# Optimization experiments

Measured on AMD Instinct MI355X. Metric: run time of the kernel, lower is better.

## Reference

```python
import jax, jax.numpy as jnp
import numpy as np

# Model dims (match init_kwargs)
D, L = 64, 262144          # data_size
G, J = 8, 8                # number of relations, dims per relation
FG = 16                    # filters (kernel_size) per relation
W = 31                     # window_size
PAD1 = (W - 1) // 2        # 15, left padding in the original code
F = G * FG                 # 128 total filters


def setup_inputs() -> dict:
    key = jax.random.key(0)
    k1, k2 = jax.random.split(key)
    x = jax.random.normal(k1, (D, L), dtype=jnp.float32)
    # original uses torch.rand for Parameter init -> uniform [0,1)
    params = jax.random.uniform(k2, (G, FG, J, W), dtype=jnp.float32)
    # dim_relation = [[0..7],[8..15],...,[56..63]] == arange reshaped
    rel_idx = jnp.arange(G * J, dtype=jnp.int32).reshape(G, J)
    return {"x": x, "params": params, "rel_idx": rel_idx}


def _forward(x, params, rel_idx):
    xg = x[rel_idx]                                   # [G, J, L] gather relation dims

    # Interior positions (PAD1 <= k <= L-W+PAD1): full-window correlation.
    # Expressed as a grouped 1D conv (lax conv is cross-correlation, matching
    # the original data*kernel elementwise-sum, no kernel flip).
    lhs = xg.reshape(1, G * J, L)                     # [N=1, C=G*J, L]
    rhs = params.reshape(G * FG, J, W)                # [O=G*FG, I=J, W]
    y = jax.lax.conv_general_dilated(
        lhs, rhs, window_strides=(1,),
        padding=[(PAD1, W - 1 - PAD1)],
        dimension_numbers=("NCH", "OIH", "NCH"),
        feature_group_count=G,
    )[0].reshape(G, FG, L)

    # Left boundary (k < PAD1): the original aligns kernel[0] with x[...,0]
    # and truncates BOTH at k+W-PAD1, i.e. y[k] = sum_{w < k+W-PAD1} xg[:, :, w]*K[..., w]
    # (NOT zero padding). Cumulative sum over w gives all prefixes at once.
    pl = jnp.einsum("gjw,gfjw->gfw", xg[:, :, :W], params)      # [G, FG, W]
    left_c = jnp.cumsum(pl, axis=-1)
    y = y.at[:, :, :PAD1].set(left_c[:, :, W - PAD1 - 1: W - 1])

    # Right boundary (k > L-W+PAD1): kernel[-1] aligned with x[..., L-1],
    # truncated at the front: y[k] = sum_{w >= W-m} xg[:, :, L-W+w]*K[..., w],
    # with m = L-k+PAD1. Reverse cumsum gives all suffixes.
    pr = jnp.einsum("gjw,gfjw->gfw", xg[:, :, L - W:], params)  # [G, FG, W]
    right_c = jnp.cumsum(pr[:, :, ::-1], axis=-1)[:, :, ::-1]    # suffix sums
    n_right = W - 1 - PAD1                                       # positions k = L-W+PAD1+1 .. L-1
    y = y.at[:, :, L - n_right:].set(right_c[:, :, 1: W - PAD1])

    return y.reshape(F * L, 1)                        # matches y.view(-1, 1)


def reference(x, params, rel_idx):
    return _forward(x, params, rel_idx)
```

## Files before the change

kernel.cpp:

```cpp
#include <hip/hip_runtime.h>

#define LL    262144
#define GG    8
#define JJ    8
#define FGF   16
#define WW    31
#define PAD1  15
#define NB    1024
#define NTHR  256
#define XTLEN (NB + 32)

typedef __bf16 bf16x8 __attribute__((ext_vector_type(8)));
typedef float  f32x4  __attribute__((ext_vector_type(4)));

__device__ inline unsigned short f2bf(float f) {
    unsigned int u = __float_as_uint(f);
    u = (u + 0x7FFF + ((u >> 16) & 1)) >> 16;
    return (unsigned short)u;
}

__global__ __launch_bounds__(NTHR, 4)
void conv_mfma(const float* __restrict__ x, const float* __restrict__ p,
               const int* __restrict__ rel, float* __restrict__ out)
{
    __shared__ unsigned short pw[32 * 16 * 8];
    __shared__ unsigned short xt[XTLEN * 8];

    const int t = threadIdx.x;
    const int g = blockIdx.y;
    const long nbase = (long)blockIdx.x * NB;

    {
        const float* pg = p + (long)g * FGF * JJ * WW;
        for (int i = t; i < FGF * JJ * WW; i += NTHR) {
            int f = i / (JJ * WW);
            int r = i - f * (JJ * WW);
            int j = r / WW;
            int w = r - j * WW;
            pw[(w * 16 + f) * 8 + j] = f2bf(pg[i]);
        }
        if (t < FGF * JJ) {
            int f = t >> 3, j = t & 7;
            pw[(31 * 16 + f) * 8 + j] = 0;
        }
    }

    {
        const int j  = t >> 5;
        const int p0 = t & 31;
        const float* xr = x + (long)rel[g * JJ + j] * LL;
        #pragma unroll
        for (int c = 0; c < XTLEN / 32; ++c) {
            int pos = c * 32 + p0;
            long gp = nbase - 16 + pos;
            float v = (gp >= 0 && gp < LL) ? xr[gp] : 0.0f;
            xt[pos * 8 + j] = f2bf(v);
        }
    }
    __syncthreads();

    const int lane = t & 63;
    const int wid  = t >> 6;
    const int col  = lane & 15;
    const int q    = lane >> 4;

    bf16x8 a[8];
    #pragma unroll
    for (int s = 0; s < 8; ++s)
        a[s] = *(const bf16x8*)&pw[((s * 4 + q) * 16 + col) * 8];

    const int pb = wid * 256 + col + q + 1;

    #define LDX(pos) (*(const bf16x8*)&xt[(pos) * 8])

    bf16x8 F00 = LDX(pb + 0), F01 = LDX(pb + 4), F02 = LDX(pb + 8), F03 = LDX(pb + 12);

    #pragma unroll
    for (int u = 0; u < 8; ++u) {
        const int o = pb + u * 32;
        bf16x8 F10 = LDX(o + 16), F11 = LDX(o + 20), F12 = LDX(o + 24), F13 = LDX(o + 28);
        bf16x8 F20 = LDX(o + 32), F21 = LDX(o + 36), F22 = LDX(o + 40), F23 = LDX(o + 44);

        f32x4 acc0 = {0.f, 0.f, 0.f, 0.f};
        f32x4 acc1 = {0.f, 0.f, 0.f, 0.f};
        acc0 = __builtin_amdgcn_mfma_f32_16x16x32_bf16(a[0], F00, acc0, 0, 0, 0);
        acc1 = __builtin_amdgcn_mfma_f32_16x16x32_bf16(a[0], F10, acc1, 0, 0, 0);
        acc0 = __builtin_amdgcn_mfma_f32_16x16x32_bf16(a[1], F01, acc0, 0, 0, 0);
        acc1 = __builtin_amdgcn_mfma_f32_16x16x32_bf16(a[1], F11, acc1, 0, 0, 0);
        acc0 = __builtin_amdgcn_mfma_f32_16x16x32_bf16(a[2], F02, acc0, 0, 0, 0);
        acc1 = __builtin_amdgcn_mfma_f32_16x16x32_bf16(a[2], F12, acc1, 0, 0, 0);
        acc0 = __builtin_amdgcn_mfma_f32_16x16x32_bf16(a[3], F03, acc0, 0, 0, 0);
        acc1 = __builtin_amdgcn_mfma_f32_16x16x32_bf16(a[3], F13, acc1, 0, 0, 0);
        acc0 = __builtin_amdgcn_mfma_f32_16x16x32_bf16(a[4], F10, acc0, 0, 0, 0);
        acc1 = __builtin_amdgcn_mfma_f32_16x16x32_bf16(a[4], F20, acc1, 0, 0, 0);
        acc0 = __builtin_amdgcn_mfma_f32_16x16x32_bf16(a[5], F11, acc0, 0, 0, 0);
        acc1 = __builtin_amdgcn_mfma_f32_16x16x32_bf16(a[5], F21, acc1, 0, 0, 0);
        acc0 = __builtin_amdgcn_mfma_f32_16x16x32_bf16(a[6], F12, acc0, 0, 0, 0);
        acc1 = __builtin_amdgcn_mfma_f32_16x16x32_bf16(a[6], F22, acc1, 0, 0, 0);
        acc0 = __builtin_amdgcn_mfma_f32_16x16x32_bf16(a[7], F13, acc0, 0, 0, 0);
        acc1 = __builtin_amdgcn_mfma_f32_16x16x32_bf16(a[7], F23, acc1, 0, 0, 0);

        const long kc0 = nbase + (long)(wid * 16 + 2 * u) * 16 + col;
        #pragma unroll
        for (int r = 0; r < 4; ++r) {
            int f = q * 4 + r;
            size_t ro = (size_t)(g * FGF + f) * LL;
            out[ro + kc0]      = acc0[r];
            out[ro + kc0 + 16] = acc1[r];
        }

        F00 = F20; F01 = F21; F02 = F22; F03 = F23;
    }
    #undef LDX
}

__global__ void conv_edges(const float* __restrict__ x, const float* __restrict__ p,
                           const int* __restrict__ rel, float* __restrict__ out)
{
    __shared__ float lp[FGF * JJ * WW];
    __shared__ float xl[JJ * WW];
    __shared__ float xr[JJ * WW];

    const int g = blockIdx.x;
    const int t = threadIdx.x;

    for (int i = t; i < FGF * JJ * WW; i += NTHR)
        lp[i] = p[(long)g * FGF * JJ * WW + i];

    for (int i = t; i < JJ * WW; i += NTHR) {
        int j = i / WW, w = i % WW;
        long row = rel[g * JJ + j];
        xl[i] = x[row * LL + w];
        xr[i] = x[row * LL + (LL - WW) + w];
    }
    __syncthreads();

    const int f  = t >> 4;
    const int qq = t & 15;
    if (qq < PAD1) {
        float a = 0.0f, b = 0.0f;
        for (int j = 0; j < JJ; ++j) {
            const float* pf  = &lp[(f * JJ + j) * WW];
            const float* xlj = &xl[j * WW];
            const float* xrj = &xr[j * WW];
            #pragma unroll
            for (int w = 0; w < WW; ++w) {
                const float pv = pf[w];
                if (w <= qq + PAD1) a += xlj[w] * pv;
                if (w >= qq + 1)    b += xrj[w] * pv;
            }
        }
        size_t rowo = (size_t)(g * FGF + f) * LL;
        out[rowo + qq] = a;
        out[rowo + (LL - PAD1) + qq] = b;
    }
}

extern "C" void kernel_launch(void* const* d_in, const int* in_sizes, int n_in,
                              void* d_out, int out_size, void* d_ws, size_t ws_size,
                              hipStream_t stream)
{
    const float* x   = (const float*)d_in[0];
    const float* p   = (const float*)d_in[1];
    const int*   rel = (const int*)d_in[2];
    float* out = (float*)d_out;

    dim3 grid(LL / NB, GG);
    conv_mfma<<<grid, NTHR, 0, stream>>>(x, p, rel, out);
    conv_edges<<<GG, NTHR, 0, stream>>>(x, p, rel, out);
}
```

Measured before the change: 239.2 us.

## Swap MFMA operands for vectorized stores, float4 loads, fuse edge kernel, halve tile

Swaps the MFMA A/B operands so each lane holds four consecutive output positions for one filter, which allows 16-byte vector stores instead of scattered scalar stores. The x tile is now loaded with float4 global reads, and the weight staging loop is rewritten to write LDS contiguously with shift-based indexing. The separate boundary kernel is folded into the first and last blocks, and the per-block tile is halved to double the block count. Together these target write coalescing, load efficiency and launch overhead. The costs are more redundant halo loads per block and the edge work serializing inside two blocks.

```diff
diff --git a/kernel.cpp b/kernel.cpp
--- a/kernel.cpp
+++ b/kernel.cpp
@@ -6,9 +6,10 @@
 #define FGF   16
 #define WW    31
 #define PAD1  15
-#define NB    1024
+#define NB    512
 #define NTHR  256
 #define XTLEN (NB + 32)
+#define NF4   (XTLEN / 4 * JJ)
 
 typedef __bf16 bf16x8 __attribute__((ext_vector_type(8)));
 typedef float  f32x4  __attribute__((ext_vector_type(4)));
@@ -32,29 +33,42 @@
 
     {
         const float* pg = p + (long)g * FGF * JJ * WW;
-        for (int i = t; i < FGF * JJ * WW; i += NTHR) {
-            int f = i / (JJ * WW);
-            int r = i - f * (JJ * WW);
-            int j = r / WW;
-            int w = r - j * WW;
-            pw[(w * 16 + f) * 8 + j] = f2bf(pg[i]);
-        }
-        if (t < FGF * JJ) {
-            int f = t >> 3, j = t & 7;
-            pw[(31 * 16 + f) * 8 + j] = 0;
+        #pragma unroll
+        for (int k = 0; k < 16; ++k) {
+            int i = t + k * NTHR;
+            int w = i >> 7;
+            int f = (i >> 3) & 15;
+            int j = i & 7;
+            float v = (w < WW) ? pg[(f * JJ + j) * WW + w] : 0.0f;
+            pw[i] = f2bf(v);
         }
     }
 
     {
-        const int j  = t >> 5;
-        const int p0 = t & 31;
-        const float* xr = x + (long)rel[g * JJ + j] * LL;
         #pragma unroll
-        for (int c = 0; c < XTLEN / 32; ++c) {
-            int pos = c * 32 + p0;
-            long gp = nbase - 16 + pos;
-            float v = (gp >= 0 && gp < LL) ? xr[gp] : 0.0f;
-            xt[pos * 8 + j] = f2bf(v);
+        for (int k = 0; k < 5; ++k) {
+            int i = t + k * NTHR;
+            if (i < NF4) {
+                int j = i / (XTLEN / 4);
+                int c = i - j * (XTLEN / 4);
+                int pos = c * 4;
+                long gp = nbase - 16 + pos;
+                const float* xr = x + (long)rel[g * JJ + j] * LL + gp;
+                float v0, v1, v2, v3;
+                if (gp >= 0 && gp + 3 < LL) {
+                    float4 v = *(const float4*)xr;
+                    v0 = v.x; v1 = v.y; v2 = v.z; v3 = v.w;
+                } else {
+                    v0 = (gp + 0 >= 0 && gp + 0 < LL) ? xr[0] : 0.0f;
+                    v1 = (gp + 1 >= 0 && gp + 1 < LL) ? xr[1] : 0.0f;
+                    v2 = (gp + 2 >= 0 && gp + 2 < LL) ? xr[2] : 0.0f;
+                    v3 = (gp + 3 >= 0 && gp + 3 < LL) ? xr[3] : 0.0f;
+                }
+                xt[(pos + 0) * 8 + j] = f2bf(v0);
+                xt[(pos + 1) * 8 + j] = f2bf(v1);
+                xt[(pos + 2) * 8 + j] = f2bf(v2);
+                xt[(pos + 3) * 8 + j] = f2bf(v3);
+            }
         }
     }
     __syncthreads();
@@ -64,95 +78,70 @@
     const int col  = lane & 15;
     const int q    = lane >> 4;
 
-    bf16x8 a[8];
+    bf16x8 b[8];
     #pragma unroll
     for (int s = 0; s < 8; ++s)
-        a[s] = *(const bf16x8*)&pw[((s * 4 + q) * 16 + col) * 8];
+        b[s] = *(const bf16x8*)&pw[((s * 4 + q) * 16 + col) * 8];
 
-    const int pb = wid * 256 + col + q + 1;
+    const int pb = wid * 128 + col + q + 1;
 
     #define LDX(pos) (*(const bf16x8*)&xt[(pos) * 8])
 
     bf16x8 F00 = LDX(pb + 0), F01 = LDX(pb + 4), F02 = LDX(pb + 8), F03 = LDX(pb + 12);
 
     #pragma unroll
-    for (int u = 0; u < 8; ++u) {
+    for (int u = 0; u < 4; ++u) {
         const int o = pb + u * 32;
         bf16x8 F10 = LDX(o + 16), F11 = LDX(o + 20), F12 = LDX(o + 24), F13 = LDX(o + 28);
         bf16x8 F20 = LDX(o + 32), F21 = LDX(o + 36), F22 = LDX(o + 40), F23 = LDX(o + 44);
 
         f32x4 acc0 = {0.f, 0.f, 0.f, 0.f};
         f32x4 acc1 = {0.f, 0.f, 0.f, 0.f};
-        acc0 = __builtin_amdgcn_mfma_f32_16x16x32_bf16(a[0], F00, acc0, 0, 0, 0);
-        acc1 = __builtin_amdgcn_mfma_f32_16x16x32_bf16(a[0], F10, acc1, 0, 0, 0);
-        acc0 = __builtin_amdgcn_mfma_f32_16x16x32_bf16(a[1], F01, acc0, 0, 0, 0);
-        acc1 = __builtin_amdgcn_mfma_f32_16x16x32_bf16(a[1], F11, acc1, 0, 0, 0);
-        acc0 = __builtin_amdgcn_mfma_f32_16x16x32_bf16(a[2], F02, acc0, 0, 0, 0);
-        acc1 = __builtin_amdgcn_mfma_f32_16x16x32_bf16(a[2], F12, acc1, 0, 0, 0);
-        acc0 = __builtin_amdgcn_mfma_f32_16x16x32_bf16(a[3], F03, acc0, 0, 0, 0);
-        acc1 = __builtin_amdgcn_mfma_f32_16x16x32_bf16(a[3], F13, acc1, 0, 0, 0);
-        acc0 = __builtin_amdgcn_mfma_f32_16x16x32_bf16(a[4], F10, acc0, 0, 0, 0);
-        acc1 = __builtin_amdgcn_mfma_f32_16x16x32_bf16(a[4], F20, acc1, 0, 0, 0);
-        acc0 = __builtin_amdgcn_mfma_f32_16x16x32_bf16(a[5], F11, acc0, 0, 0, 0);
-        acc1 = __builtin_amdgcn_mfma_f32_16x16x32_bf16(a[5], F21, acc1, 0, 0, 0);
-        acc0 = __builtin_amdgcn_mfma_f32_16x16x32_bf16(a[6], F12, acc0, 0, 0, 0);
-        acc1 = __builtin_amdgcn_mfma_f32_16x16x32_bf16(a[6], F22, acc1, 0, 0, 0);
-        acc0 = __builtin_amdgcn_mfma_f32_16x16x32_bf16(a[7], F13, acc0, 0, 0, 0);
-        acc1 = __builtin_amdgcn_mfma_f32_16x16x32_bf16(a[7], F23, acc1, 0, 0, 0);
+        acc0 = __builtin_amdgcn_mfma_f32_16x16x32_bf16(F00, b[0], acc0, 0, 0, 0);
+        acc1 = __builtin_amdgcn_mfma_f32_16x16x32_bf16(F10, b[0], acc1, 0, 0, 0);
+        acc0 = __builtin_amdgcn_mfma_f32_16x16x32_bf16(F01, b[1], acc0, 0, 0, 0);
+        acc1 = __builtin_amdgcn_mfma_f32_16x16x32_bf16(F11, b[1], acc1, 0, 0, 0);
+        acc0 = __builtin_amdgcn_mfma_f32_16x16x32_bf16(F02, b[2], acc0, 0, 0, 0);
+        acc1 = __builtin_amdgcn_mfma_f32_16x16x32_bf16(F12, b[2], acc1, 0, 0, 0);
+        acc0 = __builtin_amdgcn_mfma_f32_16x16x32_bf16(F03, b[3], acc0, 0, 0, 0);
+        acc1 = __builtin_amdgcn_mfma_f32_16x16x32_bf16(F13, b[3], acc1, 0, 0, 0);
+        acc0 = __builtin_amdgcn_mfma_f32_16x16x32_bf16(F10, b[4], acc0, 0, 0, 0);
+        acc1 = __builtin_amdgcn_mfma_f32_16x16x32_bf16(F20, b[4], acc1, 0, 0, 0);
+        acc0 = __builtin_amdgcn_mfma_f32_16x16x32_bf16(F11, b[5], acc0, 0, 0, 0);
+        acc1 = __builtin_amdgcn_mfma_f32_16x16x32_bf16(F21, b[5], acc1, 0, 0, 0);
+        acc0 = __builtin_amdgcn_mfma_f32_16x16x32_bf16(F12, b[6], acc0, 0, 0, 0);
+        acc1 = __builtin_amdgcn_mfma_f32_16x16x32_bf16(F22, b[6], acc1, 0, 0, 0);
+        acc0 = __builtin_amdgcn_mfma_f32_16x16x32_bf16(F13, b[7], acc0, 0, 0, 0);
+        acc1 = __builtin_amdgcn_mfma_f32_16x16x32_bf16(F23, b[7], acc1, 0, 0, 0);
 
-        const long kc0 = nbase + (long)(wid * 16 + 2 * u) * 16 + col;
-        #pragma unroll
-        for (int r = 0; r < 4; ++r) {
-            int f = q * 4 + r;
-            size_t ro = (size_t)(g * FGF + f) * LL;
-            out[ro + kc0]      = acc0[r];
-            out[ro + kc0 + 16] = acc1[r];
-        }
+        const long kc0 = nbase + (long)(wid * 128 + u * 32) + q * 4;
+        const size_t ro = (size_t)(g * FGF + col) * LL;
+        *(f32x4*)&out[ro + kc0]      = acc0;
+        *(f32x4*)&out[ro + kc0 + 16] = acc1;
 
         F00 = F20; F01 = F21; F02 = F22; F03 = F23;
     }
     #undef LDX
-}
 
-__global__ void conv_edges(const float* __restrict__ x, const float* __restrict__ p,
-                           const int* __restrict__ rel, float* __restrict__ out)
-{
-    __shared__ float lp[FGF * JJ * WW];
-    __shared__ float xl[JJ * WW];
-    __shared__ float xr[JJ * WW];
-
-    const int g = blockIdx.x;
-    const int t = threadIdx.x;
-
-    for (int i = t; i < FGF * JJ * WW; i += NTHR)
-        lp[i] = p[(long)g * FGF * JJ * WW + i];
-
-    for (int i = t; i < JJ * WW; i += NTHR) {
-        int j = i / WW, w = i % WW;
-        long row = rel[g * JJ + j];
-        xl[i] = x[row * LL + w];
-        xr[i] = x[row * LL + (LL - WW) + w];
-    }
-    __syncthreads();
-
-    const int f  = t >> 4;
-    const int qq = t & 15;
-    if (qq < PAD1) {
-        float a = 0.0f, b = 0.0f;
-        for (int j = 0; j < JJ; ++j) {
-            const float* pf  = &lp[(f * JJ + j) * WW];
-            const float* xlj = &xl[j * WW];
-            const float* xrj = &xr[j * WW];
-            #pragma unroll
-            for (int w = 0; w < WW; ++w) {
-                const float pv = pf[w];
-                if (w <= qq + PAD1) a += xlj[w] * pv;
-                if (w >= qq + 1)    b += xrj[w] * pv;
+    if (blockIdx.x == 0 || blockIdx.x == (LL / NB - 1)) {
+        __syncthreads();
+        const int f  = t >> 4;
+        const int qq = t & 15;
+        if (qq < PAD1) {
+            const bool left = (blockIdx.x == 0);
+            float a = 0.0f;
+            for (int j = 0; j < JJ; ++j) {
+                const float* pf = p + (((long)(g * FGF + f)) * JJ + j) * WW;
+                const float* xj = x + (long)rel[g * JJ + j] * LL + (left ? 0 : LL - WW);
+                #pragma unroll
+                for (int w = 0; w < WW; ++w) {
+                    bool use = left ? (w <= qq + PAD1) : (w >= qq + 1);
+                    if (use) a += xj[w] * pf[w];
+                }
             }
+            const size_t ro = (size_t)(g * FGF + f) * LL;
+            out[ro + (left ? (long)qq : (long)(LL - PAD1) + qq)] = a;
         }
-        size_t rowo = (size_t)(g * FGF + f) * LL;
-        out[rowo + qq] = a;
-        out[rowo + (LL - PAD1) + qq] = b;
     }
 }
 
@@ -167,5 +156,4 @@
 
     dim3 grid(LL / NB, GG);
     conv_mfma<<<grid, NTHR, 0, stream>>>(x, p, rel, out);
-    conv_edges<<<GG, NTHR, 0, stream>>>(x, p, rel, out);
 }
```

Result: no change. 236.2 us (-1.3%).
